# Kernel optimization log

Measured on AMD Instinct MI355X. Metric: run time of the kernel, lower is better.

Reference implementation:

```python
import jax, jax.numpy as jnp
import numpy as np

VOCAB = 8192
EMB = 80
UNITS = 2048
LAYERS = 6
BATCH = 64
SEQ = 64


def setup_inputs() -> dict:
    key = jax.random.key(0)
    ks = jax.random.split(key, 7)
    inputs = jax.random.randint(ks[0], (BATCH, SEQ), 0, VOCAB)
    emb = jax.random.normal(ks[1], (VOCAB, EMB), dtype=jnp.float32) * 0.05
    Wx = jax.random.normal(ks[2], (LAYERS, EMB, UNITS), dtype=jnp.float32) / np.sqrt(EMB)
    Wh = jax.random.normal(ks[3], (LAYERS, UNITS, UNITS), dtype=jnp.float32) / np.sqrt(UNITS)
    b = jnp.zeros((LAYERS, UNITS), dtype=jnp.float32)
    Wout = jax.random.normal(ks[4], (UNITS, 1), dtype=jnp.float32) / np.sqrt(UNITS)
    bout = jnp.zeros((1,), dtype=jnp.float32)
    return {"inputs": inputs, "emb": emb, "Wx": Wx, "Wh": Wh, "b": b, "Wout": Wout, "bout": bout}


def reference(inputs, emb, Wx, Wh, b, Wout, bout):
    # x: [B, T, EMB]
    x = emb[inputs]
    L = Wx.shape[0]
    B, U = inputs.shape[0], Wh.shape[-1]

    def step(states, xt):
        # states: [L, B, U]; xt: [B, EMB]
        # Faithful to original: every layer consumes xt and states[0],
        # and states[0] is updated before layers 1..L-1 read it.
        s0 = states[0]
        hs = []
        for i in range(L):
            h = jnp.tanh(xt @ Wx[i] + s0 @ Wh[i] + b[i])
            if i == 0:
                s0 = h
            hs.append(h)
        return jnp.stack(hs), None

    init = jnp.zeros((L, B, U), dtype=x.dtype)
    states, _ = jax.lax.scan(step, init, jnp.swapaxes(x, 0, 1))
    h_last = states[-1]  # last layer's output at final timestep, [B, U]
    return jax.nn.sigmoid(h_last @ Wout + bout)
```

## Files before the change

kernel.cpp:

```cpp
#include <hip/hip_runtime.h>
#include <math.h>

#define VOCABN 8192
#define EMBN   80
#define UNITSN 2048
#define BATCHN 64
#define SEQN   64

typedef _Float16 f16;
typedef _Float16 f16x8 __attribute__((ext_vector_type(8)));
typedef float    f32x4 __attribute__((ext_vector_type(4)));

#define BROW 4352

#define HBUF_BYTES   (2 * BATCHN * UNITSN * 2)
#define FLAGS_OFF    HBUF_BYTES
#define OUTPRE_OFF   (FLAGS_OFF + 4 * 64 * 4)
#define WS_ZERO_B    (OUTPRE_OFF + BATCHN * 4)

__device__ __forceinline__ f32x4 mfma16(f16x8 a, f16x8 b, f32x4 c) {
    return __builtin_amdgcn_mfma_f32_16x16x32_f16(a, b, c, 0, 0, 0);
}

__device__ __forceinline__ void bypass_load_b16(f16x8* dst, const void* p) {
    asm volatile("global_load_dwordx4 %0, %1, off sc0 sc1"
                 : "=v"(*dst) : "v"(p) : "memory");
}
__device__ __forceinline__ int bypass_load_b32(const void* p) {
    int r;
    asm volatile("global_load_dword %0, %1, off sc0 sc1\n\ts_waitcnt vmcnt(0)"
                 : "=v"(r) : "v"(p) : "memory");
    return r;
}
__device__ __forceinline__ void bypass_store_b32(void* p, unsigned int v) {
    asm volatile("global_store_dword %0, %1, off sc0 sc1"
                 :: "v"(p), "v"(v) : "memory");
}
__device__ __forceinline__ void wait_vm0(void) {
    asm volatile("s_waitcnt vmcnt(0)" ::: "memory");
    __builtin_amdgcn_sched_barrier(0);
}

__device__ __forceinline__ void load_wslice(const float* __restrict__ W,
                                            const float* __restrict__ Wxp,
                                            int c0, int tid, unsigned char* Blds)
{
    const int j0 = tid >> 3, l8 = tid & 7;
    for (int it = 0; it < 64; ++it) {
        const int j = j0 + it * 32;
        const float4 w = *(const float4*)(W + (size_t)j * UNITSN + c0 + l8 * 4);
        const float vals[4] = {w.x, w.y, w.z, w.w};
#pragma unroll
        for (int q = 0; q < 4; ++q) {
            const int uu = l8 * 4 + q;
            *(f16*)(Blds + uu * BROW + ((2 * j) ^ ((uu & 15) << 4))) = (f16)vals[q];
        }
    }
    for (int j2 = j0; j2 < 96; j2 += 32) {
        float vals[4] = {0.f, 0.f, 0.f, 0.f};
        if (j2 < EMBN) {
            const float4 w = *(const float4*)(Wxp + (size_t)j2 * UNITSN + c0 + l8 * 4);
            vals[0] = w.x; vals[1] = w.y; vals[2] = w.z; vals[3] = w.w;
        }
#pragma unroll
        for (int q = 0; q < 4; ++q) {
            const int uu = l8 * 4 + q;
            const int k = 2048 + j2;
            *(f16*)(Blds + uu * BROW + ((2 * k) ^ ((uu & 15) << 4))) = (f16)vals[q];
        }
    }
}

__global__ __launch_bounds__(256)
void rnn_recur(const int* __restrict__ inputs, const float* __restrict__ emb,
               const float* __restrict__ Wx, const float* __restrict__ Wh,
               const float* __restrict__ bias, f16* __restrict__ hbuf,
               int* __restrict__ flags)
{
    __shared__ unsigned char Blds[32 * BROW];
    __shared__ f16  xlds[2][16][96];
    __shared__ float red[4][2][64][4];
    __shared__ int  idxlds[16][SEQN];

    const int tid = threadIdx.x;
    const int wg  = blockIdx.x;
    const int g     = wg >> 6;
    const int wslot = wg & 63;
    const int c0  = wslot * 32;
    const int g16 = g * 16;

    for (int i = tid; i < 16 * SEQN; i += 256)
        idxlds[i >> 6][i & 63] = inputs[(g16 + (i >> 6)) * SEQN + (i & 63)];

    load_wslice(Wh, Wx, c0, tid, Blds);
    __syncthreads();

    {
        const int r  = tid >> 4;
        const int kb = (tid & 15) * 6;
        const float* erow = emb + (size_t)idxlds[r][0] * EMBN;
#pragma unroll
        for (int q = 0; q < 6; ++q) {
            const int k = kb + q;
            xlds[0][r][k] = (f16)((k < EMBN) ? erow[k] : 0.f);
        }
    }
    __syncthreads();

    const int lane = tid & 63;
    const int wv   = tid >> 6;
    const int l16  = lane & 15;
    const int lq   = lane >> 4;
    const int rr  = tid >> 4;
    const int cpa = (tid & 15) * 2;
    const float ba = bias[c0 + cpa];
    const float bb = bias[c0 + cpa + 1];
    const int tla = cpa >> 4;
    const int la  = ((rr >> 2) << 4) + (cpa & 15);
    const int rg  = rr & 3;

    int* gflags = flags + g * 64;

    for (int t = 0; t < SEQN; ++t) {
        const int p = t & 1;

        f32x4 acc0 = {0.f, 0.f, 0.f, 0.f};
        f32x4 acc1 = {0.f, 0.f, 0.f, 0.f};
        {
            const f16* hrow = hbuf + (size_t)p * BATCHN * UNITSN
                            + (size_t)(g16 + l16) * UNITSN + wv * 512 + lq * 8;
            const int swz = l16 << 4;
            const unsigned char* brow0 = Blds + l16 * BROW;
            const unsigned char* brow1 = Blds + (16 + l16) * BROW;
            f16x8 av[16];
#pragma unroll
            for (int kk = 0; kk < 16; ++kk)
                bypass_load_b16(&av[kk], hrow + kk * 32);
            f16x8 ax;
            if (wv < 3) ax = *(const f16x8*)(&xlds[p][l16][wv * 32 + lq * 8]);
            wait_vm0();
#pragma unroll
            for (int kk = 0; kk < 16; ++kk) {
                const int k0 = wv * 512 + kk * 32 + lq * 8;
                const int bo = (2 * k0) ^ swz;
                acc0 = mfma16(av[kk], *(const f16x8*)(brow0 + bo), acc0);
                acc1 = mfma16(av[kk], *(const f16x8*)(brow1 + bo), acc1);
            }
            if (wv < 3) {
                const int k0 = 2048 + wv * 32 + lq * 8;
                const int bo = (2 * k0) ^ swz;
                acc0 = mfma16(ax, *(const f16x8*)(brow0 + bo), acc0);
                acc1 = mfma16(ax, *(const f16x8*)(brow1 + bo), acc1);
            }
        }
        *(f32x4*)(&red[wv][0][lane][0]) = acc0;
        *(f32x4*)(&red[wv][1][lane][0]) = acc1;
        __syncthreads();

        {
            float va = ba, vb = bb;
#pragma unroll
            for (int w = 0; w < 4; ++w) {
                va += red[w][tla][la][rg];
                vb += red[w][tla][la + 1][rg];
            }
            const f16 ha = (f16)tanhf(va);
            const f16 hb = (f16)tanhf(vb);
            const unsigned int pk = (unsigned int)__builtin_bit_cast(unsigned short, ha)
                                  | ((unsigned int)__builtin_bit_cast(unsigned short, hb) << 16);
            unsigned int* dst = (unsigned int*)(hbuf + (size_t)(p ^ 1) * BATCHN * UNITSN
                                                + (size_t)(g16 + rr) * UNITSN + c0 + cpa);
            bypass_store_b32(dst, pk);
        }
        asm volatile("s_waitcnt vmcnt(0)" ::: "memory");
        __syncthreads();

        if (t == SEQN - 1) break;

        if (tid == 0)
            bypass_store_b32(&gflags[wslot], (unsigned int)(t + 1));

        {
            const int r  = tid >> 4;
            const int kb = (tid & 15) * 6;
            const float* erow = emb + (size_t)idxlds[r][t + 1] * EMBN;
            const int buf = (t + 1) & 1;
#pragma unroll
            for (int q = 0; q < 6; ++q) {
                const int k = kb + q;
                xlds[buf][r][k] = (f16)((k < EMBN) ? erow[k] : 0.f);
            }
        }

        if (wv == 0) {
            int tries = 0;
            for (;;) {
                const int v = bypass_load_b32(&gflags[lane]);
                if (__all(v > t)) break;
                __builtin_amdgcn_s_sleep(1);
                if (++tries > 150000) break;
            }
        }
        __syncthreads();
    }
}

__global__ __launch_bounds__(256)
void final_gemm(const int* __restrict__ inputs, const float* __restrict__ emb,
                const float* __restrict__ Wx, const float* __restrict__ Wh,
                const float* __restrict__ bias, const float* __restrict__ Wout,
                const f16* __restrict__ hbuf, float* __restrict__ out_pre)
{
    __shared__ unsigned char Blds[32 * BROW];
    __shared__ f16  xlds[64][96];
    __shared__ float red[4][64][4];
    __shared__ float rowacc[64][4];

    const int tid = threadIdx.x;
    const int c0  = blockIdx.x * 32;
    const float* Wh5 = Wh + (size_t)5 * UNITSN * UNITSN;
    const float* Wx5 = Wx + (size_t)5 * EMBN * UNITSN;
    const float* b5  = bias + 5 * UNITSN;

    load_wslice(Wh5, Wx5, c0, tid, Blds);
    {
        const int r  = tid >> 2;
        const int kb = (tid & 3) * 24;
        const float* erow = emb + (size_t)inputs[r * SEQN + SEQN - 1] * EMBN;
#pragma unroll
        for (int q = 0; q < 24; ++q) {
            const int k = kb + q;
            xlds[r][k] = (f16)((k < EMBN) ? erow[k] : 0.f);
        }
    }
    rowacc[tid >> 2][tid & 3] = 0.f;
    __syncthreads();

    const int lane = tid & 63;
    const int wv   = tid >> 6;
    const int l16  = lane & 15;
    const int lq   = lane >> 4;

    for (int ct = 0; ct < 2; ++ct) {
        f32x4 acc[4];
#pragma unroll
        for (int rt = 0; rt < 4; ++rt) acc[rt] = (f32x4){0.f, 0.f, 0.f, 0.f};
        const unsigned char* brow = Blds + (ct * 16 + l16) * BROW;
        const int swz = l16 << 4;
#pragma unroll
        for (int rt = 0; rt < 4; ++rt) {
            const f16* hrow = hbuf + (size_t)(rt * 16 + l16) * UNITSN + wv * 512 + lq * 8;
            f16x8 av[16];
#pragma unroll
            for (int kk = 0; kk < 16; ++kk)
                bypass_load_b16(&av[kk], hrow + kk * 32);
            f16x8 ax;
            if (wv < 3) ax = *(const f16x8*)(&xlds[rt * 16 + l16][wv * 32 + lq * 8]);
            wait_vm0();
#pragma unroll
            for (int kk = 0; kk < 16; ++kk) {
                const int k0 = wv * 512 + kk * 32 + lq * 8;
                acc[rt] = mfma16(av[kk], *(const f16x8*)(brow + ((2 * k0) ^ swz)), acc[rt]);
            }
            if (wv < 3) {
                const int k0 = 2048 + wv * 32 + lq * 8;
                acc[rt] = mfma16(ax, *(const f16x8*)(brow + ((2 * k0) ^ swz)), acc[rt]);
            }
        }
        if (wv == 0) {
#pragma unroll
            for (int rt = 0; rt < 4; ++rt) *(f32x4*)(&red[rt][lane][0]) = acc[rt];
        }
        __syncthreads();
#pragma unroll
        for (int w = 1; w < 4; ++w) {
            if (wv == w) {
#pragma unroll
                for (int rt = 0; rt < 4; ++rt) {
                    f32x4 cur = *(f32x4*)(&red[rt][lane][0]);
                    cur += acc[rt];
                    *(f32x4*)(&red[rt][lane][0]) = cur;
                }
            }
            __syncthreads();
        }
        {
            const int r = tid >> 2;
            float rsum = 0.f;
#pragma unroll
            for (int q = 0; q < 4; ++q) {
                const int cl = (tid & 3) * 4 + q;
                const int c  = ct * 16 + cl;
                const int lidx = (((r & 15) >> 2) << 4) + cl;
                float v = red[r >> 4][lidx][r & 3] + b5[c0 + c];
                v = tanhf(v);
                rsum += v * Wout[c0 + c];
            }
            rowacc[r][tid & 3] += rsum;
        }
        __syncthreads();
    }
    if (tid < 64) {
        const float s = rowacc[tid][0] + rowacc[tid][1] + rowacc[tid][2] + rowacc[tid][3];
        atomicAdd(&out_pre[tid], s);
    }
}

__global__ void final_out(const float* __restrict__ out_pre,
                          const float* __restrict__ bout, float* __restrict__ out)
{
    const int b = threadIdx.x;
    if (b < BATCHN) out[b] = 1.f / (1.f + expf(-(out_pre[b] + bout[0])));
}

extern "C" void kernel_launch(void* const* d_in, const int* in_sizes, int n_in,
                              void* d_out, int out_size, void* d_ws, size_t ws_size,
                              hipStream_t stream) {
    (void)in_sizes; (void)n_in; (void)out_size; (void)ws_size;
    const int*   inputs = (const int*)d_in[0];
    const float* emb    = (const float*)d_in[1];
    const float* Wx     = (const float*)d_in[2];
    const float* Wh     = (const float*)d_in[3];
    const float* bias   = (const float*)d_in[4];
    const float* Wout   = (const float*)d_in[5];
    const float* bout   = (const float*)d_in[6];
    float* out = (float*)d_out;

    f16*   hbuf    = (f16*)d_ws;
    int*   flags   = (int*)((char*)d_ws + FLAGS_OFF);
    float* out_pre = (float*)((char*)d_ws + OUTPRE_OFF);

    (void)hipMemsetAsync(d_ws, 0, WS_ZERO_B, stream);

    hipStreamCaptureStatus cs = hipStreamCaptureStatusNone;
    (void)hipStreamIsCapturing(stream, &cs);
    if (cs == hipStreamCaptureStatusActive) {
        rnn_recur<<<dim3(256), dim3(256), 0, stream>>>(inputs, emb, Wx, Wh, bias, hbuf, flags);
    } else {
        void* args[] = {(void*)&inputs, (void*)&emb, (void*)&Wx, (void*)&Wh,
                        (void*)&bias, (void*)&hbuf, (void*)&flags};
        hipError_t e = hipLaunchCooperativeKernel((const void*)rnn_recur, dim3(256), dim3(256),
                                                  args, 0, stream);
        if (e != hipSuccess) {
            rnn_recur<<<dim3(256), dim3(256), 0, stream>>>(inputs, emb, Wx, Wh, bias, hbuf, flags);
        }
    }
    final_gemm<<<dim3(64), dim3(256), 0, stream>>>(inputs, emb, Wx, Wh, bias, Wout, hbuf, out_pre);
    final_out<<<dim3(1), dim3(64), 0, stream>>>(out_pre, bout, out);
}
```

Before: 339.3 us.

## Store hidden state in MFMA fragment order and move flag wait before the step

Changes the hidden-state buffer to a fragment-major layout, so each lane's 16-byte A-operand load is contiguous per 1KB chunk instead of strided across rows. The embedding row for the step is now read straight from global memory into registers, which drops the xlds LDS staging and one barrier per step. The cross-workgroup flag spin now runs at the top of each step in every wave, not only wave 0 followed by a barrier. Together these aim to shorten the per-timestep critical path of the persistent recurrence. The cost is all waves polling the flags and an uncached embedding gather on every step.

New measurement: 396.9 us. 17.0% more time.

```diff
diff --git a/kernel.cpp b/kernel.cpp
--- a/kernel.cpp
+++ b/kernel.cpp
@@ -13,7 +13,7 @@
 
 #define BROW 4352
 
-#define HBUF_BYTES   (2 * BATCHN * UNITSN * 2)
+#define HBUF_BYTES   (2 * 4 * 64 * 1024)
 #define FLAGS_OFF    HBUF_BYTES
 #define OUTPRE_OFF   (FLAGS_OFF + 4 * 64 * 4)
 #define WS_ZERO_B    (OUTPRE_OFF + BATCHN * 4)
@@ -78,7 +78,6 @@
                int* __restrict__ flags)
 {
     __shared__ unsigned char Blds[32 * BROW];
-    __shared__ f16  xlds[2][16][96];
     __shared__ float red[4][2][64][4];
     __shared__ int  idxlds[16][SEQN];
 
@@ -93,18 +92,6 @@
         idxlds[i >> 6][i & 63] = inputs[(g16 + (i >> 6)) * SEQN + (i & 63)];
 
     load_wslice(Wh, Wx, c0, tid, Blds);
-    __syncthreads();
-
-    {
-        const int r  = tid >> 4;
-        const int kb = (tid & 15) * 6;
-        const float* erow = emb + (size_t)idxlds[r][0] * EMBN;
-#pragma unroll
-        for (int q = 0; q < 6; ++q) {
-            const int k = kb + q;
-            xlds[0][r][k] = (f16)((k < EMBN) ? erow[k] : 0.f);
-        }
-    }
     __syncthreads();
 
     const int lane = tid & 63;
@@ -118,26 +105,44 @@
     const int tla = cpa >> 4;
     const int la  = ((rr >> 2) << 4) + (cpa & 15);
     const int rg  = rr & 3;
-
+    const int lane_t = ((cpa >> 3) << 4) | rr;
+
+    char* hb = (char*)hbuf;
     int* gflags = flags + g * 64;
 
+    const int k0x = wv * 32 + lq * 8;
+    const bool xvalid = (wv < 3) && (k0x < EMBN);
+
     for (int t = 0; t < SEQN; ++t) {
-        const int p = t & 1;
+        if (t > 0) {
+            int tries = 0;
+            for (;;) {
+                const int v = bypass_load_b32(&gflags[lane]);
+                if (__all(v >= t)) break;
+                __builtin_amdgcn_s_sleep(1);
+                if (++tries > 150000) break;
+            }
+        }
 
         f32x4 acc0 = {0.f, 0.f, 0.f, 0.f};
         f32x4 acc1 = {0.f, 0.f, 0.f, 0.f};
         {
-            const f16* hrow = hbuf + (size_t)p * BATCHN * UNITSN
-                            + (size_t)(g16 + l16) * UNITSN + wv * 512 + lq * 8;
+            const char* hsrc = hb + (((t & 1) * 4 + g) << 16) + (lane << 4);
+            f16x8 av[16];
+#pragma unroll
+            for (int kk = 0; kk < 16; ++kk)
+                bypass_load_b16(&av[kk], hsrc + ((wv * 16 + kk) << 10));
+            f16x8 ax = {0, 0, 0, 0, 0, 0, 0, 0};
+            if (xvalid) {
+                const float* e = emb + (size_t)idxlds[l16][t] * EMBN + k0x;
+                const float4 u = *(const float4*)e;
+                const float4 w2 = *(const float4*)(e + 4);
+                ax[0] = (f16)u.x;  ax[1] = (f16)u.y;  ax[2] = (f16)u.z;  ax[3] = (f16)u.w;
+                ax[4] = (f16)w2.x; ax[5] = (f16)w2.y; ax[6] = (f16)w2.z; ax[7] = (f16)w2.w;
+            }
             const int swz = l16 << 4;
             const unsigned char* brow0 = Blds + l16 * BROW;
             const unsigned char* brow1 = Blds + (16 + l16) * BROW;
-            f16x8 av[16];
-#pragma unroll
-            for (int kk = 0; kk < 16; ++kk)
-                bypass_load_b16(&av[kk], hrow + kk * 32);
-            f16x8 ax;
-            if (wv < 3) ax = *(const f16x8*)(&xlds[p][l16][wv * 32 + lq * 8]);
             wait_vm0();
 #pragma unroll
             for (int kk = 0; kk < 16; ++kk) {
@@ -165,43 +170,18 @@
                 vb += red[w][tla][la + 1][rg];
             }
             const f16 ha = (f16)tanhf(va);
-            const f16 hb = (f16)tanhf(vb);
+            const f16 hbv = (f16)tanhf(vb);
             const unsigned int pk = (unsigned int)__builtin_bit_cast(unsigned short, ha)
-                                  | ((unsigned int)__builtin_bit_cast(unsigned short, hb) << 16);
-            unsigned int* dst = (unsigned int*)(hbuf + (size_t)(p ^ 1) * BATCHN * UNITSN
-                                                + (size_t)(g16 + rr) * UNITSN + c0 + cpa);
+                                  | ((unsigned int)__builtin_bit_cast(unsigned short, hbv) << 16);
+            char* dst = hb + ((((t + 1) & 1) * 4 + g) << 16) + (wslot << 10)
+                      + (lane_t << 4) + ((cpa & 7) << 1);
             bypass_store_b32(dst, pk);
         }
         asm volatile("s_waitcnt vmcnt(0)" ::: "memory");
         __syncthreads();
 
-        if (t == SEQN - 1) break;
-
-        if (tid == 0)
+        if (t < SEQN - 1 && tid == 0)
             bypass_store_b32(&gflags[wslot], (unsigned int)(t + 1));
-
-        {
-            const int r  = tid >> 4;
-            const int kb = (tid & 15) * 6;
-            const float* erow = emb + (size_t)idxlds[r][t + 1] * EMBN;
-            const int buf = (t + 1) & 1;
-#pragma unroll
-            for (int q = 0; q < 6; ++q) {
-                const int k = kb + q;
-                xlds[buf][r][k] = (f16)((k < EMBN) ? erow[k] : 0.f);
-            }
-        }
-
-        if (wv == 0) {
-            int tries = 0;
-            for (;;) {
-                const int v = bypass_load_b32(&gflags[lane]);
-                if (__all(v > t)) break;
-                __builtin_amdgcn_s_sleep(1);
-                if (++tries > 150000) break;
-            }
-        }
-        __syncthreads();
     }
 }
 
@@ -221,6 +201,7 @@
     const float* Wh5 = Wh + (size_t)5 * UNITSN * UNITSN;
     const float* Wx5 = Wx + (size_t)5 * EMBN * UNITSN;
     const float* b5  = bias + 5 * UNITSN;
+    const char* hb = (const char*)hbuf;
 
     load_wslice(Wh5, Wx5, c0, tid, Blds);
     {
@@ -249,14 +230,13 @@
         const int swz = l16 << 4;
 #pragma unroll
         for (int rt = 0; rt < 4; ++rt) {
-            const f16* hrow = hbuf + (size_t)(rt * 16 + l16) * UNITSN + wv * 512 + lq * 8;
+            const char* hsrc = hb + (rt << 16) + (lane << 4);
             f16x8 av[16];
 #pragma unroll
             for (int kk = 0; kk < 16; ++kk)
-                bypass_load_b16(&av[kk], hrow + kk * 32);
+                av[kk] = *(const f16x8*)(hsrc + ((wv * 16 + kk) << 10));
             f16x8 ax;
             if (wv < 3) ax = *(const f16x8*)(&xlds[rt * 16 + l16][wv * 32 + lq * 8]);
-            wait_vm0();
 #pragma unroll
             for (int kk = 0; kk < 16; ++kk) {
                 const int k0 = wv * 512 + kk * 32 + lq * 8;
```

## Hold recurrent weight slice in registers and use MFMA-fragment hidden-state layout

Applied to the files above, without the earlier changes.

The persistent recurrent kernel now runs 128 workgroups, each owning 64 output columns for a 16-row batch group. The fp16 weight slice is loaded once into per-lane register fragments (17x4 f16x8), replacing the per-step LDS reads of the weights. The hidden-state buffer is stored in a fragment-tiled layout, so each lane loads a contiguous 16-byte chunk and stores 8-byte packed results. This cuts LDS traffic and the number of workgroups that must sync each step. The cost is very high register pressure with possible spills, and fewer CUs in use, which puts more MFMA work on each one.

Result: no change. 344.5 us (+1.5%).

```diff
diff --git a/kernel.cpp b/kernel.cpp
--- a/kernel.cpp
+++ b/kernel.cpp
@@ -10,13 +10,16 @@
 typedef _Float16 f16;
 typedef _Float16 f16x8 __attribute__((ext_vector_type(8)));
 typedef float    f32x4 __attribute__((ext_vector_type(4)));
+typedef unsigned int u32x2 __attribute__((ext_vector_type(2)));
 
 #define BROW 4352
 
-#define HBUF_BYTES   (2 * BATCHN * UNITSN * 2)
+#define HBUF_BYTES   (2 * 4 * 64 * 1024)
 #define FLAGS_OFF    HBUF_BYTES
 #define OUTPRE_OFF   (FLAGS_OFF + 4 * 64 * 4)
 #define WS_ZERO_B    (OUTPRE_OFF + BATCHN * 4)
+
+#define KPW 544
 
 __device__ __forceinline__ f32x4 mfma16(f16x8 a, f16x8 b, f32x4 c) {
     return __builtin_amdgcn_mfma_f32_16x16x32_f16(a, b, c, 0, 0, 0);
@@ -36,9 +39,201 @@
     asm volatile("global_store_dword %0, %1, off sc0 sc1"
                  :: "v"(p), "v"(v) : "memory");
 }
+__device__ __forceinline__ void bypass_store_b64(void* p, u32x2 v) {
+    asm volatile("global_store_dwordx2 %0, %1, off sc0 sc1"
+                 :: "v"(p), "v"(v) : "memory");
+}
 __device__ __forceinline__ void wait_vm0(void) {
     asm volatile("s_waitcnt vmcnt(0)" ::: "memory");
     __builtin_amdgcn_sched_barrier(0);
+}
+__device__ __forceinline__ unsigned int us(f16 h) {
+    return (unsigned int)__builtin_bit_cast(unsigned short, h);
+}
+
+__global__ __launch_bounds__(256, 1)
+void rnn_recur(const int* __restrict__ inputs, const float* __restrict__ emb,
+               const float* __restrict__ Wx, const float* __restrict__ Wh,
+               const float* __restrict__ bias, f16* __restrict__ hbuf,
+               int* __restrict__ flags)
+{
+    __shared__ __align__(16) char smem[99840];
+    __shared__ f16  xlds[2][16][96];
+    __shared__ int  idxlds[16][SEQN];
+
+    const int tid = threadIdx.x;
+    const int wg  = blockIdx.x;
+    const int g     = wg >> 5;
+    const int wslot = wg & 31;
+    const int c0  = wslot * 64;
+    const int g16 = g * 16;
+
+    for (int i = tid; i < 16 * SEQN; i += 256)
+        idxlds[i >> 6][i & 63] = inputs[(g16 + (i >> 6)) * SEQN + (i & 63)];
+
+    const int lane = tid & 63;
+    const int wv   = tid >> 6;
+    const int l16  = lane & 15;
+    const int lq   = lane >> 4;
+
+    f16x8 b[17][4];
+    {
+        f16* Wtmp = (f16*)smem;
+        for (int ch = 0; ch < 3; ++ch) {
+            const int base  = ch * 768;
+            const int nrows = (base + 768 <= 2176) ? 768 : (2176 - base);
+            for (int rp = 0; rp < nrows; rp += 16) {
+                const int r_ = rp + (tid >> 4);
+                if (r_ < nrows) {
+                    const int k = base + r_;
+                    float4 w = {0.f, 0.f, 0.f, 0.f};
+                    if (k < UNITSN)
+                        w = *(const float4*)(Wh + (size_t)k * UNITSN + c0 + (tid & 15) * 4);
+                    else if (k - UNITSN < EMBN)
+                        w = *(const float4*)(Wx + (size_t)(k - UNITSN) * UNITSN + c0 + (tid & 15) * 4);
+                    f16* d = &Wtmp[r_ * 65 + (tid & 15) * 4];
+                    d[0] = (f16)w.x; d[1] = (f16)w.y; d[2] = (f16)w.z; d[3] = (f16)w.w;
+                }
+            }
+            __syncthreads();
+#pragma unroll
+            for (int i = 0; i < 17; ++i) {
+                const int k = wv * KPW + i * 32;
+                if (k >= base && k < base + 768) {
+                    const int kl = k - base + lq * 8;
+#pragma unroll
+                    for (int ct = 0; ct < 4; ++ct) {
+#pragma unroll
+                        for (int e = 0; e < 8; ++e)
+                            b[i][ct][e] = Wtmp[(kl + e) * 65 + ct * 16 + l16];
+                    }
+                }
+            }
+            __syncthreads();
+        }
+    }
+
+    {
+        const int r  = tid >> 4;
+        const int kb = (tid & 15) * 6;
+        const float* erow = emb + (size_t)idxlds[r][0] * EMBN;
+#pragma unroll
+        for (int q = 0; q < 6; ++q) {
+            const int k = kb + q;
+            xlds[0][r][k] = (f16)((k < EMBN) ? erow[k] : 0.f);
+        }
+    }
+    __syncthreads();
+
+    const int rr = tid >> 4;
+    const int cb = (tid & 15) * 4;
+    float bias4[4];
+#pragma unroll
+    for (int q = 0; q < 4; ++q) bias4[q] = bias[c0 + cb + q];
+    const int gc     = c0 + cb;
+    const int kt_p   = gc >> 5;
+    const int cc     = gc & 31;
+    const int lane_t = ((cc >> 3) << 4) | rr;
+    const int pbyte  = lane_t * 16 + (cc & 7) * 2;
+
+    char* hb = (char*)hbuf;
+    int* gflags = flags + g * 32;
+    float* red = (float*)smem;
+
+    for (int t = 0; t < SEQN; ++t) {
+        const int p = t & 1;
+
+        f32x4 acc[4];
+#pragma unroll
+        for (int ct = 0; ct < 4; ++ct) acc[ct] = (f32x4){0.f, 0.f, 0.f, 0.f};
+        {
+            const char* hsrc = hb + ((p * 4 + g) << 16) + (lane << 4);
+            f16x8 av[17];
+#pragma unroll
+            for (int i = 0; i < 17; ++i) {
+                if (wv * KPW + i * 32 < UNITSN)
+                    bypass_load_b16(&av[i], hsrc + ((wv * 17 + i) << 10));
+            }
+            f16x8 axf0 = {}, axf1 = {}, axf2 = {};
+            if (wv == 3) {
+                axf0 = *(const f16x8*)(&xlds[p][l16][0 * 32 + lq * 8]);
+                axf1 = *(const f16x8*)(&xlds[p][l16][1 * 32 + lq * 8]);
+                axf2 = *(const f16x8*)(&xlds[p][l16][2 * 32 + lq * 8]);
+            }
+            wait_vm0();
+#pragma unroll
+            for (int i = 0; i < 17; ++i) {
+                if (wv * KPW + i * 32 < UNITSN) {
+#pragma unroll
+                    for (int ct = 0; ct < 4; ++ct)
+                        acc[ct] = mfma16(av[i], b[i][ct], acc[ct]);
+                }
+            }
+            if (wv == 3) {
+#pragma unroll
+                for (int ct = 0; ct < 4; ++ct) acc[ct] = mfma16(axf0, b[13][ct], acc[ct]);
+#pragma unroll
+                for (int ct = 0; ct < 4; ++ct) acc[ct] = mfma16(axf1, b[14][ct], acc[ct]);
+#pragma unroll
+                for (int ct = 0; ct < 4; ++ct) acc[ct] = mfma16(axf2, b[15][ct], acc[ct]);
+            }
+        }
+#pragma unroll
+        for (int ct = 0; ct < 4; ++ct)
+            *(f32x4*)(&red[(((wv * 4) + ct) * 64 + lane) * 4]) = acc[ct];
+        __syncthreads();
+
+        {
+            float vv[4];
+#pragma unroll
+            for (int q = 0; q < 4; ++q) {
+                const int c  = cb + q;
+                const int tl = c >> 4;
+                const int la = ((rr >> 2) << 4) | (c & 15);
+                const int rg = rr & 3;
+                float s = bias4[q];
+#pragma unroll
+                for (int w = 0; w < 4; ++w)
+                    s += red[(((w * 4) + tl) * 64 + la) * 4 + rg];
+                vv[q] = tanhf(s);
+            }
+            u32x2 pk;
+            pk[0] = us((f16)vv[0]) | (us((f16)vv[1]) << 16);
+            pk[1] = us((f16)vv[2]) | (us((f16)vv[3]) << 16);
+            char* dst = hb + ((((t + 1) & 1) * 4 + g) << 16) + (kt_p << 10) + pbyte;
+            bypass_store_b64(dst, pk);
+        }
+        asm volatile("s_waitcnt vmcnt(0)" ::: "memory");
+        __syncthreads();
+
+        if (t == SEQN - 1) break;
+
+        if (tid == 0)
+            bypass_store_b32(&gflags[wslot], (unsigned int)(t + 1));
+
+        {
+            const int r  = tid >> 4;
+            const int kb = (tid & 15) * 6;
+            const float* erow = emb + (size_t)idxlds[r][t + 1] * EMBN;
+            const int buf = (t + 1) & 1;
+#pragma unroll
+            for (int q = 0; q < 6; ++q) {
+                const int k = kb + q;
+                xlds[buf][r][k] = (f16)((k < EMBN) ? erow[k] : 0.f);
+            }
+        }
+
+        if (wv == 0) {
+            int tries = 0;
+            for (;;) {
+                const int v = bypass_load_b32(&gflags[lane & 31]);
+                if (__all(v > t)) break;
+                __builtin_amdgcn_s_sleep(1);
+                if (++tries > 150000) break;
+            }
+        }
+        __syncthreads();
+    }
 }
 
 __device__ __forceinline__ void load_wslice(const float* __restrict__ W,
@@ -68,140 +263,6 @@
             const int k = 2048 + j2;
             *(f16*)(Blds + uu * BROW + ((2 * k) ^ ((uu & 15) << 4))) = (f16)vals[q];
         }
-    }
-}
-
-__global__ __launch_bounds__(256)
-void rnn_recur(const int* __restrict__ inputs, const float* __restrict__ emb,
-               const float* __restrict__ Wx, const float* __restrict__ Wh,
-               const float* __restrict__ bias, f16* __restrict__ hbuf,
-               int* __restrict__ flags)
-{
-    __shared__ unsigned char Blds[32 * BROW];
-    __shared__ f16  xlds[2][16][96];
-    __shared__ float red[4][2][64][4];
-    __shared__ int  idxlds[16][SEQN];
-
-    const int tid = threadIdx.x;
-    const int wg  = blockIdx.x;
-    const int g     = wg >> 6;
-    const int wslot = wg & 63;
-    const int c0  = wslot * 32;
-    const int g16 = g * 16;
-
-    for (int i = tid; i < 16 * SEQN; i += 256)
-        idxlds[i >> 6][i & 63] = inputs[(g16 + (i >> 6)) * SEQN + (i & 63)];
-
-    load_wslice(Wh, Wx, c0, tid, Blds);
-    __syncthreads();
-
-    {
-        const int r  = tid >> 4;
-        const int kb = (tid & 15) * 6;
-        const float* erow = emb + (size_t)idxlds[r][0] * EMBN;
-#pragma unroll
-        for (int q = 0; q < 6; ++q) {
-            const int k = kb + q;
-            xlds[0][r][k] = (f16)((k < EMBN) ? erow[k] : 0.f);
-        }
-    }
-    __syncthreads();
-
-    const int lane = tid & 63;
-    const int wv   = tid >> 6;
-    const int l16  = lane & 15;
-    const int lq   = lane >> 4;
-    const int rr  = tid >> 4;
-    const int cpa = (tid & 15) * 2;
-    const float ba = bias[c0 + cpa];
-    const float bb = bias[c0 + cpa + 1];
-    const int tla = cpa >> 4;
-    const int la  = ((rr >> 2) << 4) + (cpa & 15);
-    const int rg  = rr & 3;
-
-    int* gflags = flags + g * 64;
-
-    for (int t = 0; t < SEQN; ++t) {
-        const int p = t & 1;
-
-        f32x4 acc0 = {0.f, 0.f, 0.f, 0.f};
-        f32x4 acc1 = {0.f, 0.f, 0.f, 0.f};
-        {
-            const f16* hrow = hbuf + (size_t)p * BATCHN * UNITSN
-                            + (size_t)(g16 + l16) * UNITSN + wv * 512 + lq * 8;
-            const int swz = l16 << 4;
-            const unsigned char* brow0 = Blds + l16 * BROW;
-            const unsigned char* brow1 = Blds + (16 + l16) * BROW;
-            f16x8 av[16];
-#pragma unroll
-            for (int kk = 0; kk < 16; ++kk)
-                bypass_load_b16(&av[kk], hrow + kk * 32);
-            f16x8 ax;
-            if (wv < 3) ax = *(const f16x8*)(&xlds[p][l16][wv * 32 + lq * 8]);
-            wait_vm0();
-#pragma unroll
-            for (int kk = 0; kk < 16; ++kk) {
-                const int k0 = wv * 512 + kk * 32 + lq * 8;
-                const int bo = (2 * k0) ^ swz;
-                acc0 = mfma16(av[kk], *(const f16x8*)(brow0 + bo), acc0);
-                acc1 = mfma16(av[kk], *(const f16x8*)(brow1 + bo), acc1);
-            }
-            if (wv < 3) {
-                const int k0 = 2048 + wv * 32 + lq * 8;
-                const int bo = (2 * k0) ^ swz;
-                acc0 = mfma16(ax, *(const f16x8*)(brow0 + bo), acc0);
-                acc1 = mfma16(ax, *(const f16x8*)(brow1 + bo), acc1);
-            }
-        }
-        *(f32x4*)(&red[wv][0][lane][0]) = acc0;
-        *(f32x4*)(&red[wv][1][lane][0]) = acc1;
-        __syncthreads();
-
-        {
-            float va = ba, vb = bb;
-#pragma unroll
-            for (int w = 0; w < 4; ++w) {
-                va += red[w][tla][la][rg];
-                vb += red[w][tla][la + 1][rg];
-            }
-            const f16 ha = (f16)tanhf(va);
-            const f16 hb = (f16)tanhf(vb);
-            const unsigned int pk = (unsigned int)__builtin_bit_cast(unsigned short, ha)
-                                  | ((unsigned int)__builtin_bit_cast(unsigned short, hb) << 16);
-            unsigned int* dst = (unsigned int*)(hbuf + (size_t)(p ^ 1) * BATCHN * UNITSN
-                                                + (size_t)(g16 + rr) * UNITSN + c0 + cpa);
-            bypass_store_b32(dst, pk);
-        }
-        asm volatile("s_waitcnt vmcnt(0)" ::: "memory");
-        __syncthreads();
-
-        if (t == SEQN - 1) break;
-
-        if (tid == 0)
-            bypass_store_b32(&gflags[wslot], (unsigned int)(t + 1));
-
-        {
-            const int r  = tid >> 4;
-            const int kb = (tid & 15) * 6;
-            const float* erow = emb + (size_t)idxlds[r][t + 1] * EMBN;
-            const int buf = (t + 1) & 1;
-#pragma unroll
-            for (int q = 0; q < 6; ++q) {
-                const int k = kb + q;
-                xlds[buf][r][k] = (f16)((k < EMBN) ? erow[k] : 0.f);
-            }
-        }
-
-        if (wv == 0) {
-            int tries = 0;
-            for (;;) {
-                const int v = bypass_load_b32(&gflags[lane]);
-                if (__all(v > t)) break;
-                __builtin_amdgcn_s_sleep(1);
-                if (++tries > 150000) break;
-            }
-        }
-        __syncthreads();
     }
 }
 
@@ -221,6 +282,7 @@
     const float* Wh5 = Wh + (size_t)5 * UNITSN * UNITSN;
     const float* Wx5 = Wx + (size_t)5 * EMBN * UNITSN;
     const float* b5  = bias + 5 * UNITSN;
+    const char* hb = (const char*)hbuf;
 
     load_wslice(Wh5, Wx5, c0, tid, Blds);
     {
@@ -249,14 +311,13 @@
         const int swz = l16 << 4;
 #pragma unroll
         for (int rt = 0; rt < 4; ++rt) {
-            const f16* hrow = hbuf + (size_t)(rt * 16 + l16) * UNITSN + wv * 512 + lq * 8;
+            const char* hsrc = hb + (rt << 16) + (lane << 4);
             f16x8 av[16];
 #pragma unroll
             for (int kk = 0; kk < 16; ++kk)
-                bypass_load_b16(&av[kk], hrow + kk * 32);
+                av[kk] = *(const f16x8*)(hsrc + ((wv * 16 + kk) << 10));
             f16x8 ax;
             if (wv < 3) ax = *(const f16x8*)(&xlds[rt * 16 + l16][wv * 32 + lq * 8]);
-            wait_vm0();
 #pragma unroll
             for (int kk = 0; kk < 16; ++kk) {
                 const int k0 = wv * 512 + kk * 32 + lq * 8;
@@ -335,14 +396,14 @@
     hipStreamCaptureStatus cs = hipStreamCaptureStatusNone;
     (void)hipStreamIsCapturing(stream, &cs);
     if (cs == hipStreamCaptureStatusActive) {
-        rnn_recur<<<dim3(256), dim3(256), 0, stream>>>(inputs, emb, Wx, Wh, bias, hbuf, flags);
+        rnn_recur<<<dim3(128), dim3(256), 0, stream>>>(inputs, emb, Wx, Wh, bias, hbuf, flags);
     } else {
         void* args[] = {(void*)&inputs, (void*)&emb, (void*)&Wx, (void*)&Wh,
                         (void*)&bias, (void*)&hbuf, (void*)&flags};
-        hipError_t e = hipLaunchCooperativeKernel((const void*)rnn_recur, dim3(256), dim3(256),
+        hipError_t e = hipLaunchCooperativeKernel((const void*)rnn_recur, dim3(128), dim3(256),
                                                   args, 0, stream);
         if (e != hipSuccess) {
-            rnn_recur<<<dim3(256), dim3(256), 0, stream>>>(inputs, emb, Wx, Wh, bias, hbuf, flags);
+            rnn_recur<<<dim3(128), dim3(256), 0, stream>>>(inputs, emb, Wx, Wh, bias, hbuf, flags);
         }
     }
     final_gemm<<<dim3(64), dim3(256), 0, stream>>>(inputs, emb, Wx, Wh, bias, Wout, hbuf, out_pre);
```

## Replace flag barrier with epoch bits embedded in hidden-state data

Applied to the files above, without the earlier changes.

Drops the per-step flag store and the spin on flags. Each workgroup now polls the hidden-state chunks it needs directly, and readiness is detected by an epoch tag packed into the low mantissa bits of each fp16 value. The buffer grows to four rotating copies, is pre-filled with 0xFF, and the first poll uses cached loads while retries bypass the cache. This removes a barrier round trip and the extra vmcnt wait and syncthreads per step. The cost is one bit of fp16 precision, a risk of false readiness if stale data happens to match the tag, and a final GEMM that now reads the tagged values with plain loads.

Result: slower. 359.4 us (+5.9%).

```diff
diff --git a/kernel.cpp b/kernel.cpp
--- a/kernel.cpp
+++ b/kernel.cpp
@@ -6,32 +6,31 @@
 #define UNITSN 2048
 #define BATCHN 64
 #define SEQN   64
+#define RBUF   4
 
 typedef _Float16 f16;
 typedef _Float16 f16x8 __attribute__((ext_vector_type(8)));
 typedef float    f32x4 __attribute__((ext_vector_type(4)));
+typedef unsigned int u32x4 __attribute__((ext_vector_type(4)));
 
 #define BROW 4352
 
-#define HBUF_BYTES   (2 * BATCHN * UNITSN * 2)
-#define FLAGS_OFF    HBUF_BYTES
-#define OUTPRE_OFF   (FLAGS_OFF + 4 * 64 * 4)
+#define HBUF_BYTES   (RBUF * BATCHN * UNITSN * 2)
+#define OUTPRE_OFF   HBUF_BYTES
 #define WS_ZERO_B    (OUTPRE_OFF + BATCHN * 4)
 
 __device__ __forceinline__ f32x4 mfma16(f16x8 a, f16x8 b, f32x4 c) {
     return __builtin_amdgcn_mfma_f32_16x16x32_f16(a, b, c, 0, 0, 0);
 }
 
+__device__ __forceinline__ void plain_load_b16(f16x8* dst, const void* p) {
+    asm volatile("global_load_dwordx4 %0, %1, off"
+                 : "=v"(*dst) : "v"(p) : "memory");
+}
 __device__ __forceinline__ void bypass_load_b16(f16x8* dst, const void* p) {
     asm volatile("global_load_dwordx4 %0, %1, off sc0 sc1"
                  : "=v"(*dst) : "v"(p) : "memory");
 }
-__device__ __forceinline__ int bypass_load_b32(const void* p) {
-    int r;
-    asm volatile("global_load_dword %0, %1, off sc0 sc1\n\ts_waitcnt vmcnt(0)"
-                 : "=v"(r) : "v"(p) : "memory");
-    return r;
-}
 __device__ __forceinline__ void bypass_store_b32(void* p, unsigned int v) {
     asm volatile("global_store_dword %0, %1, off sc0 sc1"
                  :: "v"(p), "v"(v) : "memory");
@@ -39,6 +38,9 @@
 __device__ __forceinline__ void wait_vm0(void) {
     asm volatile("s_waitcnt vmcnt(0)" ::: "memory");
     __builtin_amdgcn_sched_barrier(0);
+}
+__device__ __forceinline__ unsigned int us(f16 h) {
+    return (unsigned int)__builtin_bit_cast(unsigned short, h);
 }
 
 __device__ __forceinline__ void load_wslice(const float* __restrict__ W,
@@ -74,8 +76,7 @@
 __global__ __launch_bounds__(256)
 void rnn_recur(const int* __restrict__ inputs, const float* __restrict__ emb,
                const float* __restrict__ Wx, const float* __restrict__ Wh,
-               const float* __restrict__ bias, f16* __restrict__ hbuf,
-               int* __restrict__ flags)
+               const float* __restrict__ bias, f16* __restrict__ hbuf)
 {
     __shared__ unsigned char Blds[32 * BROW];
     __shared__ f16  xlds[2][16][96];
@@ -119,26 +120,52 @@
     const int la  = ((rr >> 2) << 4) + (cpa & 15);
     const int rg  = rr & 3;
 
-    int* gflags = flags + g * 64;
-
     for (int t = 0; t < SEQN; ++t) {
         const int p = t & 1;
 
         f32x4 acc0 = {0.f, 0.f, 0.f, 0.f};
         f32x4 acc1 = {0.f, 0.f, 0.f, 0.f};
-        {
-            const f16* hrow = hbuf + (size_t)p * BATCHN * UNITSN
+        const int swz = l16 << 4;
+        const unsigned char* brow0 = Blds + l16 * BROW;
+        const unsigned char* brow1 = Blds + (16 + l16) * BROW;
+
+        f16x8 ax;
+        if (wv < 3) ax = *(const f16x8*)(&xlds[p][l16][wv * 32 + lq * 8]);
+
+        if (t > 0) {
+            const unsigned int e  = (unsigned)(t >> 2) & 3u;
+            const unsigned int eM = (e & 1u) | ((e & 2u) ? 0x00010000u : 0u);
+            const f16* hrow = hbuf + (size_t)(t & 3) * BATCHN * UNITSN
                             + (size_t)(g16 + l16) * UNITSN + wv * 512 + lq * 8;
-            const int swz = l16 << 4;
-            const unsigned char* brow0 = Blds + l16 * BROW;
-            const unsigned char* brow1 = Blds + (16 + l16) * BROW;
             f16x8 av[16];
-#pragma unroll
-            for (int kk = 0; kk < 16; ++kk)
-                bypass_load_b16(&av[kk], hrow + kk * 32);
-            f16x8 ax;
-            if (wv < 3) ax = *(const f16x8*)(&xlds[p][l16][wv * 32 + lq * 8]);
-            wait_vm0();
+            unsigned rdy = 0;
+            int rounds = 0;
+            for (;;) {
+#pragma unroll
+                for (int kk = 0; kk < 16; ++kk) {
+                    if (!((rdy >> kk) & 1)) {
+                        if (rounds == 0) plain_load_b16(&av[kk], hrow + kk * 32);
+                        else             bypass_load_b16(&av[kk], hrow + kk * 32);
+                    }
+                }
+                wait_vm0();
+                unsigned nrdy = rdy;
+#pragma unroll
+                for (int kk = 0; kk < 16; ++kk) {
+                    if (!((rdy >> kk) & 1)) {
+                        const u32x4 d = __builtin_bit_cast(u32x4, av[kk]);
+                        const bool ok = ((d[0] & 0x00010001u) == eM)
+                                     && ((d[1] & 0x00010001u) == eM)
+                                     && ((d[2] & 0x00010001u) == eM)
+                                     && ((d[3] & 0x00010001u) == eM);
+                        if (__all(ok)) nrdy |= (1u << kk);
+                    }
+                }
+                rdy = nrdy;
+                if (rdy == 0xFFFFu) break;
+                if (++rounds > 20000) break;
+                __builtin_amdgcn_s_sleep(1);
+            }
 #pragma unroll
             for (int kk = 0; kk < 16; ++kk) {
                 const int k0 = wv * 512 + kk * 32 + lq * 8;
@@ -146,13 +173,14 @@
                 acc0 = mfma16(av[kk], *(const f16x8*)(brow0 + bo), acc0);
                 acc1 = mfma16(av[kk], *(const f16x8*)(brow1 + bo), acc1);
             }
-            if (wv < 3) {
-                const int k0 = 2048 + wv * 32 + lq * 8;
-                const int bo = (2 * k0) ^ swz;
-                acc0 = mfma16(ax, *(const f16x8*)(brow0 + bo), acc0);
-                acc1 = mfma16(ax, *(const f16x8*)(brow1 + bo), acc1);
-            }
-        }
+        }
+        if (wv < 3) {
+            const int k0 = 2048 + wv * 32 + lq * 8;
+            const int bo = (2 * k0) ^ swz;
+            acc0 = mfma16(ax, *(const f16x8*)(brow0 + bo), acc0);
+            acc1 = mfma16(ax, *(const f16x8*)(brow1 + bo), acc1);
+        }
+
         *(f32x4*)(&red[wv][0][lane][0]) = acc0;
         *(f32x4*)(&red[wv][1][lane][0]) = acc1;
         __syncthreads();
@@ -164,23 +192,18 @@
                 va += red[w][tla][la][rg];
                 vb += red[w][tla][la + 1][rg];
             }
-            const f16 ha = (f16)tanhf(va);
-            const f16 hb = (f16)tanhf(vb);
-            const unsigned int pk = (unsigned int)__builtin_bit_cast(unsigned short, ha)
-                                  | ((unsigned int)__builtin_bit_cast(unsigned short, hb) << 16);
-            unsigned int* dst = (unsigned int*)(hbuf + (size_t)(p ^ 1) * BATCHN * UNITSN
-                                                + (size_t)(g16 + rr) * UNITSN + c0 + cpa);
+            const f16 ha  = (f16)tanhf(va);
+            const f16 hbv = (f16)tanhf(vb);
+            const unsigned int ep = (unsigned)((t + 1) >> 2) & 3u;
+            const unsigned int pk = ((us(ha)  & 0xFFFEu) | (ep & 1u))
+                                  | (((us(hbv) & 0xFFFEu) | ((ep >> 1) & 1u)) << 16);
+            unsigned int* dst = (unsigned int*)(hbuf
+                                + (size_t)((t + 1) & 3) * BATCHN * UNITSN
+                                + (size_t)(g16 + rr) * UNITSN + c0 + cpa);
             bypass_store_b32(dst, pk);
         }
-        asm volatile("s_waitcnt vmcnt(0)" ::: "memory");
-        __syncthreads();
-
-        if (t == SEQN - 1) break;
-
-        if (tid == 0)
-            bypass_store_b32(&gflags[wslot], (unsigned int)(t + 1));
-
-        {
+
+        if (t < SEQN - 1) {
             const int r  = tid >> 4;
             const int kb = (tid & 15) * 6;
             const float* erow = emb + (size_t)idxlds[r][t + 1] * EMBN;
@@ -189,16 +212,6 @@
             for (int q = 0; q < 6; ++q) {
                 const int k = kb + q;
                 xlds[buf][r][k] = (f16)((k < EMBN) ? erow[k] : 0.f);
-            }
-        }
-
-        if (wv == 0) {
-            int tries = 0;
-            for (;;) {
-                const int v = bypass_load_b32(&gflags[lane]);
-                if (__all(v > t)) break;
-                __builtin_amdgcn_s_sleep(1);
-                if (++tries > 150000) break;
             }
         }
         __syncthreads();
@@ -253,10 +266,9 @@
             f16x8 av[16];
 #pragma unroll
             for (int kk = 0; kk < 16; ++kk)
-                bypass_load_b16(&av[kk], hrow + kk * 32);
+                av[kk] = *(const f16x8*)(hrow + kk * 32);
             f16x8 ax;
             if (wv < 3) ax = *(const f16x8*)(&xlds[rt * 16 + l16][wv * 32 + lq * 8]);
-            wait_vm0();
 #pragma unroll
             for (int kk = 0; kk < 16; ++kk) {
                 const int k0 = wv * 512 + kk * 32 + lq * 8;
@@ -327,22 +339,22 @@
     float* out = (float*)d_out;
 
     f16*   hbuf    = (f16*)d_ws;
-    int*   flags   = (int*)((char*)d_ws + FLAGS_OFF);
     float* out_pre = (float*)((char*)d_ws + OUTPRE_OFF);
 
-    (void)hipMemsetAsync(d_ws, 0, WS_ZERO_B, stream);
+    (void)hipMemsetAsync(d_ws, 0xFF, HBUF_BYTES, stream);
+    (void)hipMemsetAsync((char*)d_ws + OUTPRE_OFF, 0x00, WS_ZERO_B - OUTPRE_OFF, stream);
 
     hipStreamCaptureStatus cs = hipStreamCaptureStatusNone;
     (void)hipStreamIsCapturing(stream, &cs);
     if (cs == hipStreamCaptureStatusActive) {
-        rnn_recur<<<dim3(256), dim3(256), 0, stream>>>(inputs, emb, Wx, Wh, bias, hbuf, flags);
+        rnn_recur<<<dim3(256), dim3(256), 0, stream>>>(inputs, emb, Wx, Wh, bias, hbuf);
     } else {
         void* args[] = {(void*)&inputs, (void*)&emb, (void*)&Wx, (void*)&Wh,
-                        (void*)&bias, (void*)&hbuf, (void*)&flags};
+                        (void*)&bias, (void*)&hbuf};
         hipError_t e = hipLaunchCooperativeKernel((const void*)rnn_recur, dim3(256), dim3(256),
                                                   args, 0, stream);
         if (e != hipSuccess) {
-            rnn_recur<<<dim3(256), dim3(256), 0, stream>>>(inputs, emb, Wx, Wh, bias, hbuf, flags);
+            rnn_recur<<<dim3(256), dim3(256), 0, stream>>>(inputs, emb, Wx, Wh, bias, hbuf);
         }
     }
     final_gemm<<<dim3(64), dim3(256), 0, stream>>>(inputs, emb, Wx, Wh, bias, Wout, hbuf, out_pre);
```
